# Kernel optimization log

Hardware: AMD Instinct MI355X
Metric: run time of the kernel (lower is better)

## Reference

```python
import jax, jax.numpy as jnp
import numpy as np

B, T, C, H = 2, 2048, 1024, 16  # batch, seq, n_embd, n_head


def setup_inputs() -> dict:
    key = jax.random.key(0)
    k1, k2, k3 = jax.random.split(key, 3)
    scale = 0.02
    return {
        "x": jax.random.normal(k1, (B, T, C), dtype=jnp.float32),
        "W_attn": jax.random.normal(k2, (3 * C, C), dtype=jnp.float32) * scale,
        "b_attn": jnp.zeros((3 * C,), dtype=jnp.float32),
        "W_proj": jax.random.normal(k3, (C, C), dtype=jnp.float32) * scale,
        "b_proj": jnp.zeros((C,), dtype=jnp.float32),
        "alpha": jnp.asarray(1.0, dtype=jnp.float32),
        "beta": jnp.asarray(0.1, dtype=jnp.float32),
        "gamma": jnp.asarray(0.1, dtype=jnp.float32),
    }


def reference(x, W_attn, b_attn, W_proj, b_proj, alpha, beta, gamma):
    Bx, Tx, Cx = x.shape
    d = Cx // H  # head dim
    qkv = x @ W_attn.T + b_attn                      # [B,T,3C]
    q, k, v = jnp.split(qkv, 3, axis=-1)

    def to_heads(t):
        return t.reshape(Bx, Tx, H, d).transpose(0, 2, 1, 3)  # [B,H,T,d]

    q, k, v = to_heads(q), to_heads(k), to_heads(v)

    inv_sqrt_d = jnp.asarray(1.0 / np.sqrt(d), dtype=x.dtype)
    scores = jnp.einsum('bhtd,bhsd->bhts', q, k) * inv_sqrt_d  # [B,H,T,T]

    causal = jnp.tril(jnp.ones((Tx, Tx), dtype=bool))
    scores = jnp.where(causal, scores, -jnp.inf)
    att = jax.nn.softmax(scores, axis=-1)

    # Id buffer = softmax(10000*eye) == identity; MC buffer = softmax(10000*tril)
    # == uniform causal prefix average: MC[i, j<=i] = 1/(i+1).
    id_m = jnp.eye(Tx, dtype=x.dtype)
    mc = causal.astype(x.dtype) / jnp.arange(1, Tx + 1, dtype=x.dtype)[:, None]

    shaped = beta * att + alpha * id_m - gamma * mc  # dropout p=0 -> identity
    y = jnp.einsum('bhts,bhsd->bhtd', shaped, v)     # [B,H,T,d]
    y = y.transpose(0, 2, 1, 3).reshape(Bx, Tx, Cx)
    return y @ W_proj.T + b_proj
```

## Files before the change

kernel.cpp:

```cpp
#include <hip/hip_runtime.h>
#include <stdint.h>

#define Bsz  2
#define Tseq 2048
#define Cemb 1024
#define NH   16
#define HD   64

typedef __attribute__((ext_vector_type(8))) __bf16 bf16x8;
typedef __attribute__((ext_vector_type(4))) float  f32x4;
typedef __attribute__((ext_vector_type(8))) unsigned short u16x8;

#define MFMA16(a, b, c) __builtin_amdgcn_mfma_f32_16x16x32_bf16((a), (b), (c), 0, 0, 0)

__device__ __forceinline__ unsigned short f2bf(float f) {
  union { float f; unsigned int u; } v; v.f = f;
  unsigned int u = v.u;
  u += 0x7fffu + ((u >> 16) & 1u);
  return (unsigned short)(u >> 16);
}
__device__ __forceinline__ float bf2f(unsigned short h) {
  union { unsigned int u; float f; } v; v.u = ((unsigned int)h) << 16;
  return v.f;
}
__device__ __forceinline__ unsigned int pack_bf2(float a, float b) {
  union { float f; unsigned int u; } va, vb; va.f = a; vb.f = b;
  return __builtin_amdgcn_perm(vb.u + 0x8000u, va.u + 0x8000u, 0x07060302u);
}

typedef __attribute__((address_space(1))) const unsigned int GU;
typedef __attribute__((address_space(3))) unsigned int LU;
__device__ __forceinline__ void load_lds16(const void* g, void* l) {
  __builtin_amdgcn_global_load_lds((GU*)g, (LU*)l, 16, 0, 0);
}

#define XE  4194304
#define WAE 3145728
__global__ void cast3_kernel(const float* __restrict__ x,
                             const float* __restrict__ wa,
                             const float* __restrict__ wp,
                             unsigned short* __restrict__ out) {
  const int i = (blockIdx.x * blockDim.x + threadIdx.x) * 4;
  const float* src;
  int off;
  if (i < XE) { src = x; off = i; }
  else if (i < XE + WAE) { src = wa; off = i - XE; }
  else { src = wp; off = i - (XE + WAE); }
  const float4 f = *(const float4*)(src + off);
  ushort4 o;
  o.x = f2bf(f.x); o.y = f2bf(f.y); o.z = f2bf(f.z); o.w = f2bf(f.w);
  *(ushort4*)(out + i) = o;
}

__global__ __launch_bounds__(256) void gemm_qkv_kernel(
    const unsigned short* __restrict__ A,
    const unsigned short* __restrict__ Bw,
    const float* __restrict__ bias,
    unsigned short* __restrict__ qkv,
    unsigned short* __restrict__ vt) {
  const int K = Cemb;
  __shared__ unsigned short sA[128 * 32];
  __shared__ unsigned short sB[128 * 32];
  const int tid = threadIdx.x;
  const int wave = tid >> 6, lane = tid & 63;
  const int quad = lane >> 4, lrow = lane & 15;
  const int l7 = lrow & 7;
  const int wm = (wave >> 1) * 64, wn = (wave & 1) * 64;
  const int tileM = blockIdx.y * 128, tileN = blockIdx.x * 128;

  f32x4 acc[4][4];
#pragma unroll
  for (int i = 0; i < 4; ++i)
#pragma unroll
    for (int j = 0; j < 4; ++j) acc[i][j] = (f32x4){0.f, 0.f, 0.f, 0.f};

  for (int k0 = 0; k0 < K; k0 += 32) {
    __syncthreads();
#pragma unroll
    for (int s = 0; s < 2; ++s) {
      const int cid = tid + s * 256;
      const int r = cid >> 2, ko = (cid & 3) * 8;
      load_lds16(&A[(size_t)(tileM + r) * K + k0 + ko], &sA[cid * 8]);
      load_lds16(&Bw[(size_t)(tileN + r) * K + k0 + ko], &sB[cid * 8]);
    }
    __syncthreads();
    bf16x8 af[4], bfm[4];
#pragma unroll
    for (int mt = 0; mt < 4; ++mt)
      af[mt] = *(const bf16x8*)&sA[(wm + mt * 16 + lrow) * 32 + quad * 8];
#pragma unroll
    for (int nt = 0; nt < 4; ++nt)
      bfm[nt] = *(const bf16x8*)&sB[(wn + nt * 16 + lrow) * 32 + quad * 8];
#pragma unroll
    for (int mt = 0; mt < 4; ++mt)
#pragma unroll
      for (int nt = 0; nt < 4; ++nt)
        acc[mt][nt] = MFMA16(af[mt], bfm[nt], acc[mt][nt]);
  }

  __syncthreads();
  unsigned short* sEp = sA + wave * 1024;
  float bias_v[4];
#pragma unroll
  for (int nt = 0; nt < 4; ++nt) bias_v[nt] = bias[tileN + wn + nt * 16 + lrow];
  const int gn0 = tileN + wn;
  const int part = gn0 >> 10, h = (gn0 & 1023) >> 6;

#pragma unroll
  for (int mt = 0; mt < 4; ++mt) {
#pragma unroll
    for (int nt = 0; nt < 4; ++nt)
#pragma unroll
      for (int reg = 0; reg < 4; ++reg) {
        const int q = quad * 4 + reg;
        const int ch = (nt * 2 + (lrow >> 3)) ^ (q & 7);
        sEp[q * 64 + ch * 8 + l7] = f2bf(acc[mt][nt][reg] + bias_v[nt]);
      }
    __builtin_amdgcn_wave_barrier();
#pragma unroll
    for (int i = 0; i < 2; ++i) {
      const int c = i * 64 + lane;
      const int r = c >> 3, ch2 = c & 7;
      const u16x8 row = *(const u16x8*)&sEp[r * 64 + ((ch2 ^ (r & 7)) << 3)];
      const int gm = tileM + wm + mt * 16 + r;
      const int bb = gm >> 11, t = gm & 2047;
      *(u16x8*)&qkv[((((size_t)part * Bsz + bb) * NH + h) * Tseq + t) * HD + ch2 * 8] = row;
    }
    if (part == 2) {
      unsigned int w[8];
#pragma unroll
      for (int q = 0; q < 16; q += 2) {
        const unsigned short a0 =
            sEp[q * 64 + (((lane >> 3) ^ (q & 7)) << 3) + (lane & 7)];
        const unsigned short a1 =
            sEp[(q + 1) * 64 + (((lane >> 3) ^ ((q + 1) & 7)) << 3) + (lane & 7)];
        w[q >> 1] = (unsigned int)a0 | ((unsigned int)a1 << 16);
      }
      const int gm0 = tileM + wm + mt * 16;
      const int bb = gm0 >> 11, t0 = gm0 & 2047;
      unsigned short* dst = &vt[(((size_t)bb * NH + h) * HD + lane) * Tseq + t0];
      *(uint4*)(dst) = *(const uint4*)&w[0];
      *(uint4*)(dst + 8) = *(const uint4*)&w[4];
    }
    __builtin_amdgcn_wave_barrier();
  }
}

__global__ __launch_bounds__(256) void gemm_proj_kernel(
    const unsigned short* __restrict__ A,
    const unsigned short* __restrict__ Bw,
    const float* __restrict__ bias,
    float* __restrict__ out) {
  const int K = Cemb;
  __shared__ unsigned short sA[64 * 32];
  __shared__ unsigned short sB[128 * 32];
  const int tid = threadIdx.x;
  const int wave = tid >> 6, lane = tid & 63;
  const int quad = lane >> 4, lrow = lane & 15;
  const int wn = wave * 32;
  const int tileM = blockIdx.y * 64, tileN = blockIdx.x * 128;

  f32x4 acc[4][2];
#pragma unroll
  for (int i = 0; i < 4; ++i)
#pragma unroll
    for (int j = 0; j < 2; ++j) acc[i][j] = (f32x4){0.f, 0.f, 0.f, 0.f};

  for (int k0 = 0; k0 < K; k0 += 32) {
    __syncthreads();
    {
      const int rA = tid >> 2, koA = (tid & 3) * 8;
      load_lds16(&A[(size_t)(tileM + rA) * K + k0 + koA], &sA[tid * 8]);
#pragma unroll
      for (int s = 0; s < 2; ++s) {
        const int cB = tid + s * 256;
        const int rB = cB >> 2, koB = (cB & 3) * 8;
        load_lds16(&Bw[(size_t)(tileN + rB) * K + k0 + koB], &sB[cB * 8]);
      }
    }
    __syncthreads();
    bf16x8 af[4], bfm[2];
#pragma unroll
    for (int mt = 0; mt < 4; ++mt)
      af[mt] = *(const bf16x8*)&sA[(mt * 16 + lrow) * 32 + quad * 8];
#pragma unroll
    for (int nt = 0; nt < 2; ++nt)
      bfm[nt] = *(const bf16x8*)&sB[(wn + nt * 16 + lrow) * 32 + quad * 8];
#pragma unroll
    for (int mt = 0; mt < 4; ++mt)
#pragma unroll
      for (int nt = 0; nt < 2; ++nt)
        acc[mt][nt] = MFMA16(af[mt], bfm[nt], acc[mt][nt]);
  }

#pragma unroll
  for (int mt = 0; mt < 4; ++mt)
#pragma unroll
    for (int nt = 0; nt < 2; ++nt)
#pragma unroll
      for (int reg = 0; reg < 4; ++reg) {
        const int gm = tileM + mt * 16 + quad * 4 + reg;
        const int gn = tileN + wn + nt * 16 + lrow;
        out[(size_t)gm * Cemb + gn] = acc[mt][nt][reg] + bias[gn];
      }
}

__global__ __launch_bounds__(256) void attn_kernel(
    const unsigned short* __restrict__ qkv,
    const unsigned short* __restrict__ vt,
    const float* __restrict__ palpha, const float* __restrict__ pbeta,
    const float* __restrict__ pgamma,
    unsigned short* __restrict__ y) {
  __shared__ unsigned short sK[2][64 * 64];
  __shared__ unsigned short sVt[2][64 * 64];

  const int tid = threadIdx.x;
  const int wave = tid >> 6, lane = tid & 63;
  const int quad = lane >> 4, lrow = lane & 15;
  const int bh = blockIdx.y;
  const int b = bh >> 4, h = bh & 15;

  const size_t partStride = (size_t)Bsz * NH * Tseq * HD;
  const size_t headoff = (size_t)bh * Tseq * HD;
  const unsigned short* Q = qkv + headoff;
  const unsigned short* Kp = qkv + partStride + headoff;
  const unsigned short* Vp = qkv + 2 * partStride + headoff;
  const unsigned short* Vt_g = vt + (size_t)bh * HD * Tseq;

  const float alpha = palpha[0], beta = pbeta[0], gamma = pgamma[0];
  const float SCL = 0.125f * 1.44269504089f;

  union { unsigned short u[8]; bf16x8 v; } onesU;
#pragma unroll
  for (int j = 0; j < 8; ++j) onesU.u[j] = 0x3F80;
  const bf16x8 onesF = onesU.v;

  const int qtA = blockIdx.x;
  const int qtB = 31 - qtA;
  const int q0A = qtA * 64, q0B = qtB * 64;

  const int qrowA = q0A + wave * 16 + lrow;
  const int qrowB = q0B + wave * 16 + lrow;
  const bf16x8 bQA0 = *(const bf16x8*)&Q[(size_t)qrowA * HD + quad * 8];
  const bf16x8 bQA1 = *(const bf16x8*)&Q[(size_t)qrowA * HD + 32 + quad * 8];
  const bf16x8 bQB0 = *(const bf16x8*)&Q[(size_t)qrowB * HD + quad * 8];
  const bf16x8 bQB1 = *(const bf16x8*)&Q[(size_t)qrowB * HD + 32 + quad * 8];

  const int prow = ((lrow & 12) << 1) | (lrow & 3);

  f32x4 OtA[4], UtA[4], LA, OtB[4], UtB[4], LB;
#pragma unroll
  for (int dt = 0; dt < 4; ++dt) {
    OtA[dt] = (f32x4){0.f, 0.f, 0.f, 0.f};
    UtA[dt] = (f32x4){0.f, 0.f, 0.f, 0.f};
    OtB[dt] = (f32x4){0.f, 0.f, 0.f, 0.f};
    UtB[dt] = (f32x4){0.f, 0.f, 0.f, 0.f};
  }
  LA = (f32x4){0.f, 0.f, 0.f, 0.f};
  LB = (f32x4){0.f, 0.f, 0.f, 0.f};

  auto stage_tile = [&](int it, int buf) {
    const int j0 = it * 64;
#pragma unroll
    for (int s = 0; s < 2; ++s) {
      const int c = tid + s * 256;
      const int r = c >> 3, cc = c & 7;
      const int pk = cc ^ (r & 7) ^ ((r & 16) >> 2);
      load_lds16(&Kp[(size_t)(j0 + r) * HD + pk * 8], &sK[buf][c * 8]);
      load_lds16(&Vt_g[(size_t)r * Tseq + j0 + pk * 8], &sVt[buf][c * 8]);
    }
  };

  stage_tile(0, 0);

  const int ntiles = qtB + 1;
  for (int it = 0; it < ntiles; ++it) {
    const int cur = it & 1;
    __syncthreads();
    if (it + 1 < ntiles) stage_tile(it + 1, (it + 1) & 1);

    const unsigned short* K_ = sK[cur];
    const unsigned short* Vt_ = sVt[cur];
    const int j0 = it * 64;
    const bool actA = (it <= qtA);
    const bool diagA = (it == qtA), diagB = (it == qtB);

    unsigned int pkA[4][2], pkB[4][2];
#pragma unroll
    for (int ct = 0; ct < 4; ++ct) {
      const int srow = (ct >> 1) * 32 + (ct & 1) * 4 + prow;
      const int hs = (srow & 7) ^ ((srow & 16) >> 2);
      const bf16x8 a0 = *(const bf16x8*)&K_[srow * 64 + ((quad ^ hs) << 3)];
      const bf16x8 a1 = *(const bf16x8*)&K_[srow * 64 + (((4 + quad) ^ hs) << 3)];
      const int sbase = j0 + (ct >> 1) * 32 + (ct & 1) * 4 + quad * 8;

      f32x4 sB = (f32x4){0.f, 0.f, 0.f, 0.f};
      sB = MFMA16(a0, bQB0, sB);
      sB = MFMA16(a1, bQB1, sB);
      float pB[4];
      if (diagB) {
#pragma unroll
        for (int reg = 0; reg < 4; ++reg)
          pB[reg] = exp2f((sbase + reg > qrowB) ? -1e30f : sB[reg] * SCL);
      } else {
#pragma unroll
        for (int reg = 0; reg < 4; ++reg) pB[reg] = exp2f(sB[reg] * SCL);
      }
      pkB[ct][0] = pack_bf2(pB[0], pB[1]);
      pkB[ct][1] = pack_bf2(pB[2], pB[3]);

      if (actA) {
        f32x4 sA = (f32x4){0.f, 0.f, 0.f, 0.f};
        sA = MFMA16(a0, bQA0, sA);
        sA = MFMA16(a1, bQA1, sA);
        float pA[4];
        if (diagA) {
#pragma unroll
          for (int reg = 0; reg < 4; ++reg)
            pA[reg] = exp2f((sbase + reg > qrowA) ? -1e30f : sA[reg] * SCL);
        } else {
#pragma unroll
          for (int reg = 0; reg < 4; ++reg) pA[reg] = exp2f(sA[reg] * SCL);
        }
        pkA[ct][0] = pack_bf2(pA[0], pA[1]);
        pkA[ct][1] = pack_bf2(pA[2], pA[3]);
      }
    }

    union { unsigned int w[4]; bf16x8 v; } tu;
    tu.w[0] = pkB[0][0]; tu.w[1] = pkB[0][1]; tu.w[2] = pkB[1][0]; tu.w[3] = pkB[1][1];
    const bf16x8 P1B = tu.v;
    tu.w[0] = pkB[2][0]; tu.w[1] = pkB[2][1]; tu.w[2] = pkB[3][0]; tu.w[3] = pkB[3][1];
    const bf16x8 P2B = tu.v;
    bf16x8 P1A = onesF, P2A = onesF;
    if (actA) {
      tu.w[0] = pkA[0][0]; tu.w[1] = pkA[0][1]; tu.w[2] = pkA[1][0]; tu.w[3] = pkA[1][1];
      P1A = tu.v;
      tu.w[0] = pkA[2][0]; tu.w[1] = pkA[2][1]; tu.w[2] = pkA[3][0]; tu.w[3] = pkA[3][1];
      P2A = tu.v;
    }

    LB = MFMA16(onesF, P1B, LB);
    LB = MFMA16(onesF, P2B, LB);
    if (actA) {
      LA = MFMA16(onesF, P1A, LA);
      LA = MFMA16(onesF, P2A, LA);
    }

    bf16x8 u1B = onesF, u2B = onesF, u1A = onesF, u2A = onesF;
    if (diagB) {
      union { unsigned short u[8]; bf16x8 v; } m0, m1;
#pragma unroll
      for (int jj = 0; jj < 8; ++jj) {
        m0.u[jj] = (j0 + quad * 8 + jj) <= qrowB ? (unsigned short)0x3F80 : (unsigned short)0;
        m1.u[jj] = (j0 + 32 + quad * 8 + jj) <= qrowB ? (unsigned short)0x3F80 : (unsigned short)0;
      }
      u1B = m0.v; u2B = m1.v;
    }
    if (actA && diagA) {
      union { unsigned short u[8]; bf16x8 v; } m0, m1;
#pragma unroll
      for (int jj = 0; jj < 8; ++jj) {
        m0.u[jj] = (j0 + quad * 8 + jj) <= qrowA ? (unsigned short)0x3F80 : (unsigned short)0;
        m1.u[jj] = (j0 + 32 + quad * 8 + jj) <= qrowA ? (unsigned short)0x3F80 : (unsigned short)0;
      }
      u1A = m0.v; u2A = m1.v;
    }

#pragma unroll
    for (int dt = 0; dt < 4; ++dt) {
      const int vr = dt * 16 + lrow;
      const int hvr = (vr & 7) ^ ((vr & 16) >> 2);
      const bf16x8 av0 = *(const bf16x8*)&Vt_[vr * 64 + ((quad ^ hvr) << 3)];
      const bf16x8 av1 = *(const bf16x8*)&Vt_[vr * 64 + (((4 + quad) ^ hvr) << 3)];
      OtB[dt] = MFMA16(av0, P1B, OtB[dt]);
      OtB[dt] = MFMA16(av1, P2B, OtB[dt]);
      UtB[dt] = MFMA16(av0, u1B, UtB[dt]);
      UtB[dt] = MFMA16(av1, u2B, UtB[dt]);
      if (actA) {
        OtA[dt] = MFMA16(av0, P1A, OtA[dt]);
        OtA[dt] = MFMA16(av1, P2A, OtA[dt]);
        UtA[dt] = MFMA16(av0, u1A, UtA[dt]);
        UtA[dt] = MFMA16(av1, u2A, UtA[dt]);
      }
    }
  }

  auto epilogue = [&](const f32x4* Ot, const f32x4* Ut, const f32x4& L, int qrow) {
    const float bl = beta / L[0];
    const float gi = gamma / (float)(qrow + 1);
    const size_t ybase = ((size_t)b * Tseq + qrow) * Cemb + h * HD;
#pragma unroll
    for (int dt = 0; dt < 4; ++dt) {
      const int d0 = dt * 16 + quad * 4;
      const ushort4 vv4 = *(const ushort4*)&Vp[(size_t)qrow * HD + d0];
      const unsigned short vu[4] = {vv4.x, vv4.y, vv4.z, vv4.w};
      ushort4 o;
      unsigned short* op = (unsigned short*)&o;
#pragma unroll
      for (int reg = 0; reg < 4; ++reg) {
        const float yv = bl * Ot[dt][reg] + alpha * bf2f(vu[reg]) - gi * Ut[dt][reg];
        op[reg] = f2bf(yv);
      }
      *(ushort4*)&y[ybase + d0] = o;
    }
  };
  epilogue(OtA, UtA, LA, qrowA);
  epilogue(OtB, UtB, LB, qrowB);
}

extern "C" void kernel_launch(void* const* d_in, const int* in_sizes, int n_in,
                              void* d_out, int out_size, void* d_ws, size_t ws_size,
                              hipStream_t stream) {
  const float* x  = (const float*)d_in[0];
  const float* Wa = (const float*)d_in[1];
  const float* ba = (const float*)d_in[2];
  const float* Wp = (const float*)d_in[3];
  const float* bp = (const float*)d_in[4];
  const float* alpha = (const float*)d_in[5];
  const float* beta  = (const float*)d_in[6];
  const float* gamma = (const float*)d_in[7];
  float* out = (float*)d_out;

  unsigned short* ws = (unsigned short*)d_ws;
  unsigned short* xb   = ws;
  unsigned short* wab  = xb + (size_t)XE;
  unsigned short* wpb  = wab + (size_t)WAE;
  unsigned short* qkvb = wpb + (size_t)1024 * 1024;
  unsigned short* yb   = qkvb + (size_t)3 * Bsz * NH * Tseq * HD;
  unsigned short* vtb  = yb + (size_t)Bsz * Tseq * Cemb;

  cast3_kernel<<<(XE + WAE + 1048576) / 4 / 256, 256, 0, stream>>>(x, Wa, Wp, xb);

  gemm_qkv_kernel<<<dim3(3072 / 128, 4096 / 128), 256, 0, stream>>>(xb, wab, ba, qkvb, vtb);
  attn_kernel<<<dim3(16, Bsz * NH), 256, 0, stream>>>(qkvb, vtb, alpha, beta, gamma, yb);
  gemm_proj_kernel<<<dim3(1024 / 128, 4096 / 64), 256, 0, stream>>>(yb, wpb, bp, out);
}
```

Before: 199.7 us.

## Stage 128-key tiles per barrier in attention and halve proj GEMM M-tile

The attention kernel now stages two 64-key tiles (128 keys) of K and V^T per double-buffer step, which halves the number of block barriers and enlarges each async load batch. LDS use grows to 64 KB. The output projection GEMM moves from 64-row to 32-row M tiles, doubling the grid to fill more CUs, at the cost of reloading the weight tile more often and leaving half the threads idle during A loads.

```diff
diff --git a/kernel.cpp b/kernel.cpp
--- a/kernel.cpp
+++ b/kernel.cpp
@@ -152,49 +152,49 @@
     const float* __restrict__ bias,
     float* __restrict__ out) {
   const int K = Cemb;
-  __shared__ unsigned short sA[64 * 32];
+  __shared__ unsigned short sA[32 * 32];
   __shared__ unsigned short sB[128 * 32];
   const int tid = threadIdx.x;
   const int wave = tid >> 6, lane = tid & 63;
   const int quad = lane >> 4, lrow = lane & 15;
   const int wn = wave * 32;
-  const int tileM = blockIdx.y * 64, tileN = blockIdx.x * 128;
-
-  f32x4 acc[4][2];
-#pragma unroll
-  for (int i = 0; i < 4; ++i)
+  const int tileM = blockIdx.y * 32, tileN = blockIdx.x * 128;
+
+  f32x4 acc[2][2];
+#pragma unroll
+  for (int i = 0; i < 2; ++i)
 #pragma unroll
     for (int j = 0; j < 2; ++j) acc[i][j] = (f32x4){0.f, 0.f, 0.f, 0.f};
 
   for (int k0 = 0; k0 < K; k0 += 32) {
     __syncthreads();
-    {
-      const int rA = tid >> 2, koA = (tid & 3) * 8;
-      load_lds16(&A[(size_t)(tileM + rA) * K + k0 + koA], &sA[tid * 8]);
-#pragma unroll
-      for (int s = 0; s < 2; ++s) {
-        const int cB = tid + s * 256;
-        const int rB = cB >> 2, koB = (cB & 3) * 8;
-        load_lds16(&Bw[(size_t)(tileN + rB) * K + k0 + koB], &sB[cB * 8]);
-      }
+    if (tid < 128) {
+      const int r = tid >> 2, ko = (tid & 3) * 8;
+      load_lds16(&A[(size_t)(tileM + r) * K + k0 + ko], &sA[tid * 8]);
+    }
+#pragma unroll
+    for (int s = 0; s < 2; ++s) {
+      const int cB = tid + s * 256;
+      const int rB = cB >> 2, koB = (cB & 3) * 8;
+      load_lds16(&Bw[(size_t)(tileN + rB) * K + k0 + koB], &sB[cB * 8]);
     }
     __syncthreads();
-    bf16x8 af[4], bfm[2];
-#pragma unroll
-    for (int mt = 0; mt < 4; ++mt)
+    bf16x8 af[2], bfm[2];
+#pragma unroll
+    for (int mt = 0; mt < 2; ++mt)
       af[mt] = *(const bf16x8*)&sA[(mt * 16 + lrow) * 32 + quad * 8];
 #pragma unroll
     for (int nt = 0; nt < 2; ++nt)
       bfm[nt] = *(const bf16x8*)&sB[(wn + nt * 16 + lrow) * 32 + quad * 8];
 #pragma unroll
-    for (int mt = 0; mt < 4; ++mt)
+    for (int mt = 0; mt < 2; ++mt)
 #pragma unroll
       for (int nt = 0; nt < 2; ++nt)
         acc[mt][nt] = MFMA16(af[mt], bfm[nt], acc[mt][nt]);
   }
 
 #pragma unroll
-  for (int mt = 0; mt < 4; ++mt)
+  for (int mt = 0; mt < 2; ++mt)
 #pragma unroll
     for (int nt = 0; nt < 2; ++nt)
 #pragma unroll
@@ -211,8 +211,8 @@
     const float* __restrict__ palpha, const float* __restrict__ pbeta,
     const float* __restrict__ pgamma,
     unsigned short* __restrict__ y) {
-  __shared__ unsigned short sK[2][64 * 64];
-  __shared__ unsigned short sVt[2][64 * 64];
+  __shared__ unsigned short sK[2][128 * 64];
+  __shared__ unsigned short sVt[2][64 * 128];
 
   const int tid = threadIdx.x;
   const int wave = tid >> 6, lane = tid & 63;
@@ -259,129 +259,142 @@
   LA = (f32x4){0.f, 0.f, 0.f, 0.f};
   LB = (f32x4){0.f, 0.f, 0.f, 0.f};
 
-  auto stage_tile = [&](int it, int buf) {
-    const int j0 = it * 64;
-#pragma unroll
-    for (int s = 0; s < 2; ++s) {
+  auto stage_tile = [&](int ip, int buf) {
+    const int j0 = ip * 128;
+#pragma unroll
+    for (int s = 0; s < 4; ++s) {
       const int c = tid + s * 256;
       const int r = c >> 3, cc = c & 7;
       const int pk = cc ^ (r & 7) ^ ((r & 16) >> 2);
       load_lds16(&Kp[(size_t)(j0 + r) * HD + pk * 8], &sK[buf][c * 8]);
+    }
+#pragma unroll
+    for (int s = 0; s < 4; ++s) {
+      const int c = tid + s * 256;
+      const int r = c >> 4, cc = c & 15;
+      const int pk = (cc & 8) | ((cc & 7) ^ (r & 7) ^ ((r & 16) >> 2));
       load_lds16(&Vt_g[(size_t)r * Tseq + j0 + pk * 8], &sVt[buf][c * 8]);
     }
   };
 
   stage_tile(0, 0);
 
-  const int ntiles = qtB + 1;
-  for (int it = 0; it < ntiles; ++it) {
-    const int cur = it & 1;
+  const int npairs = (qtB + 2) >> 1;
+  for (int ip = 0; ip < npairs; ++ip) {
+    const int cur = ip & 1;
     __syncthreads();
-    if (it + 1 < ntiles) stage_tile(it + 1, (it + 1) & 1);
-
-    const unsigned short* K_ = sK[cur];
-    const unsigned short* Vt_ = sVt[cur];
-    const int j0 = it * 64;
-    const bool actA = (it <= qtA);
-    const bool diagA = (it == qtA), diagB = (it == qtB);
-
-    unsigned int pkA[4][2], pkB[4][2];
-#pragma unroll
-    for (int ct = 0; ct < 4; ++ct) {
-      const int srow = (ct >> 1) * 32 + (ct & 1) * 4 + prow;
-      const int hs = (srow & 7) ^ ((srow & 16) >> 2);
-      const bf16x8 a0 = *(const bf16x8*)&K_[srow * 64 + ((quad ^ hs) << 3)];
-      const bf16x8 a1 = *(const bf16x8*)&K_[srow * 64 + (((4 + quad) ^ hs) << 3)];
-      const int sbase = j0 + (ct >> 1) * 32 + (ct & 1) * 4 + quad * 8;
-
-      f32x4 sB = (f32x4){0.f, 0.f, 0.f, 0.f};
-      sB = MFMA16(a0, bQB0, sB);
-      sB = MFMA16(a1, bQB1, sB);
-      float pB[4];
+    if (ip + 1 < npairs) stage_tile(ip + 1, (ip + 1) & 1);
+
+    const unsigned short* Kb = sK[cur];
+    const unsigned short* Vb = sVt[cur];
+
+#pragma unroll
+    for (int sub = 0; sub < 2; ++sub) {
+      const int tt = ip * 2 + sub;
+      if (tt > qtB) continue;
+      const unsigned short* K_ = Kb + sub * 64 * 64;
+      const int j0 = tt * 64;
+      const bool actA = (tt <= qtA);
+      const bool diagA = (tt == qtA), diagB = (tt == qtB);
+
+      unsigned int pkA[4][2], pkB[4][2];
+#pragma unroll
+      for (int ct = 0; ct < 4; ++ct) {
+        const int srow = (ct >> 1) * 32 + (ct & 1) * 4 + prow;
+        const int hs = (srow & 7) ^ ((srow & 16) >> 2);
+        const bf16x8 a0 = *(const bf16x8*)&K_[srow * 64 + ((quad ^ hs) << 3)];
+        const bf16x8 a1 = *(const bf16x8*)&K_[srow * 64 + (((4 + quad) ^ hs) << 3)];
+        const int sbase = j0 + (ct >> 1) * 32 + (ct & 1) * 4 + quad * 8;
+
+        f32x4 sB = (f32x4){0.f, 0.f, 0.f, 0.f};
+        sB = MFMA16(a0, bQB0, sB);
+        sB = MFMA16(a1, bQB1, sB);
+        float pB[4];
+        if (diagB) {
+#pragma unroll
+          for (int reg = 0; reg < 4; ++reg)
+            pB[reg] = exp2f((sbase + reg > qrowB) ? -1e30f : sB[reg] * SCL);
+        } else {
+#pragma unroll
+          for (int reg = 0; reg < 4; ++reg) pB[reg] = exp2f(sB[reg] * SCL);
+        }
+        pkB[ct][0] = pack_bf2(pB[0], pB[1]);
+        pkB[ct][1] = pack_bf2(pB[2], pB[3]);
+
+        if (actA) {
+          f32x4 sA = (f32x4){0.f, 0.f, 0.f, 0.f};
+          sA = MFMA16(a0, bQA0, sA);
+          sA = MFMA16(a1, bQA1, sA);
+          float pA[4];
+          if (diagA) {
+#pragma unroll
+            for (int reg = 0; reg < 4; ++reg)
+              pA[reg] = exp2f((sbase + reg > qrowA) ? -1e30f : sA[reg] * SCL);
+          } else {
+#pragma unroll
+            for (int reg = 0; reg < 4; ++reg) pA[reg] = exp2f(sA[reg] * SCL);
+          }
+          pkA[ct][0] = pack_bf2(pA[0], pA[1]);
+          pkA[ct][1] = pack_bf2(pA[2], pA[3]);
+        }
+      }
+
+      union { unsigned int w[4]; bf16x8 v; } tu;
+      tu.w[0] = pkB[0][0]; tu.w[1] = pkB[0][1]; tu.w[2] = pkB[1][0]; tu.w[3] = pkB[1][1];
+      const bf16x8 P1B = tu.v;
+      tu.w[0] = pkB[2][0]; tu.w[1] = pkB[2][1]; tu.w[2] = pkB[3][0]; tu.w[3] = pkB[3][1];
+      const bf16x8 P2B = tu.v;
+      bf16x8 P1A = onesF, P2A = onesF;
+      if (actA) {
+        tu.w[0] = pkA[0][0]; tu.w[1] = pkA[0][1]; tu.w[2] = pkA[1][0]; tu.w[3] = pkA[1][1];
+        P1A = tu.v;
+        tu.w[0] = pkA[2][0]; tu.w[1] = pkA[2][1]; tu.w[2] = pkA[3][0]; tu.w[3] = pkA[3][1];
+        P2A = tu.v;
+      }
+
+      LB = MFMA16(onesF, P1B, LB);
+      LB = MFMA16(onesF, P2B, LB);
+      if (actA) {
+        LA = MFMA16(onesF, P1A, LA);
+        LA = MFMA16(onesF, P2A, LA);
+      }
+
+      bf16x8 u1B = onesF, u2B = onesF, u1A = onesF, u2A = onesF;
       if (diagB) {
-#pragma unroll
-        for (int reg = 0; reg < 4; ++reg)
-          pB[reg] = exp2f((sbase + reg > qrowB) ? -1e30f : sB[reg] * SCL);
-      } else {
-#pragma unroll
-        for (int reg = 0; reg < 4; ++reg) pB[reg] = exp2f(sB[reg] * SCL);
-      }
-      pkB[ct][0] = pack_bf2(pB[0], pB[1]);
-      pkB[ct][1] = pack_bf2(pB[2], pB[3]);
-
-      if (actA) {
-        f32x4 sA = (f32x4){0.f, 0.f, 0.f, 0.f};
-        sA = MFMA16(a0, bQA0, sA);
-        sA = MFMA16(a1, bQA1, sA);
-        float pA[4];
-        if (diagA) {
-#pragma unroll
-          for (int reg = 0; reg < 4; ++reg)
-            pA[reg] = exp2f((sbase + reg > qrowA) ? -1e30f : sA[reg] * SCL);
-        } else {
-#pragma unroll
-          for (int reg = 0; reg < 4; ++reg) pA[reg] = exp2f(sA[reg] * SCL);
+        union { unsigned short u[8]; bf16x8 v; } m0, m1;
+#pragma unroll
+        for (int jj = 0; jj < 8; ++jj) {
+          m0.u[jj] = (j0 + quad * 8 + jj) <= qrowB ? (unsigned short)0x3F80 : (unsigned short)0;
+          m1.u[jj] = (j0 + 32 + quad * 8 + jj) <= qrowB ? (unsigned short)0x3F80 : (unsigned short)0;
         }
-        pkA[ct][0] = pack_bf2(pA[0], pA[1]);
-        pkA[ct][1] = pack_bf2(pA[2], pA[3]);
-      }
-    }
-
-    union { unsigned int w[4]; bf16x8 v; } tu;
-    tu.w[0] = pkB[0][0]; tu.w[1] = pkB[0][1]; tu.w[2] = pkB[1][0]; tu.w[3] = pkB[1][1];
-    const bf16x8 P1B = tu.v;
-    tu.w[0] = pkB[2][0]; tu.w[1] = pkB[2][1]; tu.w[2] = pkB[3][0]; tu.w[3] = pkB[3][1];
-    const bf16x8 P2B = tu.v;
-    bf16x8 P1A = onesF, P2A = onesF;
-    if (actA) {
-      tu.w[0] = pkA[0][0]; tu.w[1] = pkA[0][1]; tu.w[2] = pkA[1][0]; tu.w[3] = pkA[1][1];
-      P1A = tu.v;
-      tu.w[0] = pkA[2][0]; tu.w[1] = pkA[2][1]; tu.w[2] = pkA[3][0]; tu.w[3] = pkA[3][1];
-      P2A = tu.v;
-    }
-
-    LB = MFMA16(onesF, P1B, LB);
-    LB = MFMA16(onesF, P2B, LB);
-    if (actA) {
-      LA = MFMA16(onesF, P1A, LA);
-      LA = MFMA16(onesF, P2A, LA);
-    }
-
-    bf16x8 u1B = onesF, u2B = onesF, u1A = onesF, u2A = onesF;
-    if (diagB) {
-      union { unsigned short u[8]; bf16x8 v; } m0, m1;
-#pragma unroll
-      for (int jj = 0; jj < 8; ++jj) {
-        m0.u[jj] = (j0 + quad * 8 + jj) <= qrowB ? (unsigned short)0x3F80 : (unsigned short)0;
-        m1.u[jj] = (j0 + 32 + quad * 8 + jj) <= qrowB ? (unsigned short)0x3F80 : (unsigned short)0;
-      }
-      u1B = m0.v; u2B = m1.v;
-    }
-    if (actA && diagA) {
-      union { unsigned short u[8]; bf16x8 v; } m0, m1;
-#pragma unroll
-      for (int jj = 0; jj < 8; ++jj) {
-        m0.u[jj] = (j0 + quad * 8 + jj) <= qrowA ? (unsigned short)0x3F80 : (unsigned short)0;
-        m1.u[jj] = (j0 + 32 + quad * 8 + jj) <= qrowA ? (unsigned short)0x3F80 : (unsigned short)0;
-      }
-      u1A = m0.v; u2A = m1.v;
-    }
-
-#pragma unroll
-    for (int dt = 0; dt < 4; ++dt) {
-      const int vr = dt * 16 + lrow;
-      const int hvr = (vr & 7) ^ ((vr & 16) >> 2);
-      const bf16x8 av0 = *(const bf16x8*)&Vt_[vr * 64 + ((quad ^ hvr) << 3)];
-      const bf16x8 av1 = *(const bf16x8*)&Vt_[vr * 64 + (((4 + quad) ^ hvr) << 3)];
-      OtB[dt] = MFMA16(av0, P1B, OtB[dt]);
-      OtB[dt] = MFMA16(av1, P2B, OtB[dt]);
-      UtB[dt] = MFMA16(av0, u1B, UtB[dt]);
-      UtB[dt] = MFMA16(av1, u2B, UtB[dt]);
-      if (actA) {
-        OtA[dt] = MFMA16(av0, P1A, OtA[dt]);
-        OtA[dt] = MFMA16(av1, P2A, OtA[dt]);
-        UtA[dt] = MFMA16(av0, u1A, UtA[dt]);
-        UtA[dt] = MFMA16(av1, u2A, UtA[dt]);
+        u1B = m0.v; u2B = m1.v;
+      }
+      if (actA && diagA) {
+        union { unsigned short u[8]; bf16x8 v; } m0, m1;
+#pragma unroll
+        for (int jj = 0; jj < 8; ++jj) {
+          m0.u[jj] = (j0 + quad * 8 + jj) <= qrowA ? (unsigned short)0x3F80 : (unsigned short)0;
+          m1.u[jj] = (j0 + 32 + quad * 8 + jj) <= qrowA ? (unsigned short)0x3F80 : (unsigned short)0;
+        }
+        u1A = m0.v; u2A = m1.v;
+      }
+
+#pragma unroll
+      for (int dt = 0; dt < 4; ++dt) {
+        const int vr = dt * 16 + lrow;
+        const int hvr = (vr & 7) ^ ((vr & 16) >> 2);
+        const bf16x8 av0 = *(const bf16x8*)&Vb[vr * 128 + ((sub * 8 + (quad ^ hvr)) << 3)];
+        const bf16x8 av1 = *(const bf16x8*)&Vb[vr * 128 + ((sub * 8 + ((4 + quad) ^ hvr)) << 3)];
+        OtB[dt] = MFMA16(av0, P1B, OtB[dt]);
+        OtB[dt] = MFMA16(av1, P2B, OtB[dt]);
+        UtB[dt] = MFMA16(av0, u1B, UtB[dt]);
+        UtB[dt] = MFMA16(av1, u2B, UtB[dt]);
+        if (actA) {
+          OtA[dt] = MFMA16(av0, P1A, OtA[dt]);
+          OtA[dt] = MFMA16(av1, P2A, OtA[dt]);
+          UtA[dt] = MFMA16(av0, u1A, UtA[dt]);
+          UtA[dt] = MFMA16(av1, u2A, UtA[dt]);
+        }
       }
     }
   }
@@ -434,5 +447,5 @@
 
   gemm_qkv_kernel<<<dim3(3072 / 128, 4096 / 128), 256, 0, stream>>>(xb, wab, ba, qkvb, vtb);
   attn_kernel<<<dim3(16, Bsz * NH), 256, 0, stream>>>(qkvb, vtb, alpha, beta, gamma, yb);
-  gemm_proj_kernel<<<dim3(1024 / 128, 4096 / 64), 256, 0, stream>>>(yb, wpb, bp, out);
-}
+  gemm_proj_kernel<<<dim3(1024 / 128, 4096 / 32), 256, 0, stream>>>(yb, wpb, bp, out);
+}
```

Result: slower. 252.1 us (+26.2%).
